# Optimization experiments

Measured on AMD Instinct MI355X. Metric: run time of the kernel, lower is better.

Reference implementation:

```python
import jax, jax.numpy as jnp
import numpy as np

N_NODES = 100000
IN_CH = 256
EMBED = 256
N_EDGES = 300000
EPS = 1e-5


def _glorot(key, shape):
    fan_in, fan_out = shape[0], shape[1]
    lim = (6.0 / (fan_in + fan_out)) ** 0.5
    return jax.random.uniform(key, shape, jnp.float32, -lim, lim)


def setup_inputs() -> dict:
    key = jax.random.key(0)
    ks = jax.random.split(key, 16)
    inp = {}
    inp['node_feat'] = jax.random.normal(ks[0], (N_NODES, IN_CH), jnp.float32)
    inp['src'] = jax.random.randint(ks[1], (N_EDGES,), 0, N_NODES, jnp.int32)
    inp['dst'] = jax.random.randint(ks[2], (N_EDGES,), 0, N_NODES, jnp.int32)
    inp['neg'] = jax.random.randint(ks[3], (N_EDGES,), 0, N_NODES, jnp.int32)
    # GCNConv weights (x @ W + b), 3 layers
    inp['W1'] = _glorot(ks[4], (IN_CH, EMBED)); inp['b1'] = jnp.zeros((EMBED,), jnp.float32)
    inp['W2'] = _glorot(ks[5], (EMBED, EMBED)); inp['b2'] = jnp.zeros((EMBED,), jnp.float32)
    inp['W3'] = _glorot(ks[6], (EMBED, EMBED)); inp['b3'] = jnp.zeros((EMBED,), jnp.float32)
    # BatchNorm affine params (2 BN layers)
    inp['g1'] = jnp.ones((EMBED,), jnp.float32); inp['be1'] = jnp.zeros((EMBED,), jnp.float32)
    inp['g2'] = jnp.ones((EMBED,), jnp.float32); inp['be2'] = jnp.zeros((EMBED,), jnp.float32)
    # LinkPredictor MLP
    inp['fc1_w'] = _glorot(ks[7], (2 * EMBED, EMBED)); inp['fc1_b'] = jnp.zeros((EMBED,), jnp.float32)
    inp['fc2_w'] = _glorot(ks[8], (EMBED, 1)); inp['fc2_b'] = jnp.zeros((1,), jnp.float32)
    return inp


def gcn_conv(x, W, b, src, dst, n):
    # PyG GCNConv: out = D^{-1/2} (A + I) D^{-1/2} (x @ W) + b
    xw = x @ W
    loops = jnp.arange(n, dtype=src.dtype)
    src_l = jnp.concatenate([src, loops])
    dst_l = jnp.concatenate([dst, loops])
    deg = jax.ops.segment_sum(jnp.ones_like(dst_l, jnp.float32), dst_l, num_segments=n)
    dinv = jnp.where(deg > 0, jax.lax.rsqrt(deg), 0.0)
    norm = dinv[src_l] * dinv[dst_l]  # [E+N]
    msg = norm[:, None] * xw[src_l]   # [E+N, d]
    out = jax.ops.segment_sum(msg, dst_l, num_segments=n)
    return out + b


def batch_norm(x, g, b):
    # training-mode BN over node dim, biased variance (torch semantics)
    mu = jnp.mean(x, axis=0)
    var = jnp.mean((x - mu) ** 2, axis=0)
    return (x - mu) * jax.lax.rsqrt(var + EPS) * g + b


def link_pred(z_a, z_b, fc1_w, fc1_b, fc2_w, fc2_b):
    h = jnp.concatenate([z_a, z_b], axis=1) @ fc1_w + fc1_b
    h = jax.nn.relu(h)
    return jax.nn.sigmoid(h @ fc2_w + fc2_b).reshape(-1)


def reference(node_feat, src, dst, neg, W1, b1, W2, b2, W3, b3, g1, be1, g2, be2, fc1_w, fc1_b, fc2_w, fc2_b):
    n = node_feat.shape[0]
    # encoder (dropout p used only in training; inference/deterministic here)
    x = gcn_conv(node_feat, W1, b1, src, dst, n)
    x = jax.nn.relu(batch_norm(x, g1, be1))
    x = gcn_conv(x, W2, b2, src, dst, n)
    x = jax.nn.relu(batch_norm(x, g2, be2))
    z = gcn_conv(x, W3, b3, src, dst, n)
    z_src, z_dst, z_neg = z[src], z[dst], z[neg]
    pos_out = link_pred(z_src, z_dst, fc1_w, fc1_b, fc2_w, fc2_b)
    neg_out = link_pred(z_src, z_neg, fc1_w, fc1_b, fc2_w, fc2_b)
    return (pos_out, neg_out)
```

## Files before the change

### kernel.cpp

```cpp
#include <hip/hip_runtime.h>
#include <hip/hip_bf16.h>

#define N_NODES 100000
#define N_EDGES 300000
#define CH 256
#define EPS 1e-5f
#define AGG_BLOCKS 3125
#define Y_TILES 782
#define Y_TILES_PAD 784

typedef __hip_bfloat16 bf16;
typedef __attribute__((ext_vector_type(8))) short bf16x8_t;
typedef __attribute__((ext_vector_type(4))) float f32x4_t;

__device__ __forceinline__ unsigned short f2bf(float f) {
    bf16 h = __float2bfloat16(f);
    return __builtin_bit_cast(unsigned short, h);
}
__device__ __forceinline__ float bflo(unsigned int w) {
    return __builtin_bit_cast(float, w << 16);
}
__device__ __forceinline__ float bfhi(unsigned int w) {
    return __builtin_bit_cast(float, w & 0xffff0000u);
}
__device__ __forceinline__ unsigned pack2(float a, float b) {
    return (unsigned)f2bf(a) | ((unsigned)f2bf(b) << 16);
}
__device__ __forceinline__ void store_val(bf16* p, float v) { *p = __float2bfloat16(v); }

__device__ __forceinline__ void async_copy16(const void* g, void* l) {
    __builtin_amdgcn_global_load_lds((const __attribute__((address_space(1))) void*)g,
                                     (__attribute__((address_space(3))) void*)l, 16, 0, 0);
}

__global__ void k_zero_int(int* __restrict__ p, int n) {
    int i = blockIdx.x * 256 + threadIdx.x;
    if (i < n) p[i] = 0;
}
__global__ void k_count_deg(const int* __restrict__ dst, int* __restrict__ deg) {
    int e = blockIdx.x * 256 + threadIdx.x;
    if (e < N_EDGES) atomicAdd(&deg[dst[e]], 1);
}
__global__ void k_block_sums(const int* __restrict__ deg, int* __restrict__ bsum,
                             float* __restrict__ dinv) {
    __shared__ int s[256];
    int t = threadIdx.x;
    int i = blockIdx.x * 256 + t;
    int v = (i < N_NODES) ? deg[i] : 0;
    s[t] = v;
    if (i < N_NODES) dinv[i] = rsqrtf((float)(v + 1));
    __syncthreads();
    for (int off = 128; off > 0; off >>= 1) {
        if (t < off) s[t] += s[t + off];
        __syncthreads();
    }
    if (t == 0) bsum[blockIdx.x] = s[0];
}
__global__ void k_scan_bsums(int* __restrict__ bsum, int nb) {
    __shared__ int s[512];
    int t = threadIdx.x;
    int v = (t < nb) ? bsum[t] : 0;
    s[t] = v;
    __syncthreads();
    for (int off = 1; off < 512; off <<= 1) {
        int u = (t >= off) ? s[t - off] : 0;
        __syncthreads();
        s[t] += u;
        __syncthreads();
    }
    if (t < nb) bsum[t] = s[t] - v;
}
__global__ void k_row_ptr(const int* __restrict__ deg, const int* __restrict__ bsum,
                          int* __restrict__ row_ptr) {
    __shared__ int s[256];
    int t = threadIdx.x;
    int i = blockIdx.x * 256 + t;
    int v = (i < N_NODES) ? deg[i] : 0;
    s[t] = v;
    __syncthreads();
    for (int off = 1; off < 256; off <<= 1) {
        int u = (t >= off) ? s[t - off] : 0;
        __syncthreads();
        s[t] += u;
        __syncthreads();
    }
    if (i < N_NODES) row_ptr[i] = bsum[blockIdx.x] + s[t] - v;
    if (blockIdx.x == 0 && t == 0) row_ptr[N_NODES] = N_EDGES;
}
__global__ void k_scatter(const int* __restrict__ src, const int* __restrict__ dst,
                          const int* __restrict__ row_ptr, int* __restrict__ cursor,
                          const float* __restrict__ dinv,
                          int* __restrict__ col, float* __restrict__ wedge,
                          int* __restrict__ eid, int* __restrict__ rowid) {
    int e = blockIdx.x * 256 + threadIdx.x;
    if (e < N_EDGES) {
        int d = dst[e], s = src[e];
        int p = atomicAdd(&cursor[d], 1);
        int idx = row_ptr[d] + p;
        col[idx] = s;
        wedge[idx] = dinv[d] * dinv[s];
        eid[idx] = e;
        rowid[idx] = d;
    }
}

__global__ void k_transpose_all(const float* __restrict__ W1, const float* __restrict__ W2,
                                bf16* __restrict__ wt) {
    int which = blockIdx.x >> 8;
    int idx = ((blockIdx.x & 255) << 8) + threadIdx.x;
    int n = idx >> 8, k = idx & 255;
    const float* W = which ? W2 : W1;
    wt[(size_t)which * 65536 + (size_t)n * 256 + k] =
        __float2bfloat16(W[(size_t)k * 256 + n]);
}

__global__ void k_fuse_w(const float* __restrict__ W3, const float* __restrict__ fc1w,
                         const float* __restrict__ b3, const float* __restrict__ fc1b,
                         bf16* __restrict__ wtf, float* __restrict__ bout) {
    int n = threadIdx.x;
    int nc = n & 255;
    size_t ro = (n < 256) ? 0 : 256;
    if (blockIdx.x == 256) {
        float acc = (n < 256) ? fc1b[n] : 0.f;
#pragma unroll 4
        for (int j = 0; j < 256; ++j)
            acc += b3[j] * fc1w[(ro + j) * 256 + nc];
        bout[n] = acc;
        return;
    }
    __shared__ float w3row[256];
    int k = blockIdx.x;
    if (n < 256) w3row[n] = W3[(size_t)k * 256 + n];
    __syncthreads();
    float acc = 0.f;
#pragma unroll 4
    for (int j = 0; j < 256; ++j)
        acc += w3row[j] * fc1w[(ro + j) * 256 + nc];
    wtf[(size_t)n * 256 + k] = __float2bfloat16(acc);
}

template <int NX, bool BIAS, bool STATS, bool F32A>
__global__ __launch_bounds__(256) void k_gemm_mfma(const bf16* __restrict__ A,
                                                   const float* __restrict__ Af,
                                                   const bf16* __restrict__ Bt,
                                                   bf16* __restrict__ C, int M, int ldc,
                                                   const float* __restrict__ bias,
                                                   float* __restrict__ part) {
    constexpr int LOG2NX = (NX == 4) ? 2 : 1;
    int id = blockIdx.x;
    int rg = (id & 7) + 8 * (id >> (3 + LOG2NX));
    int ct = (id >> 3) & (NX - 1);
    if (rg >= Y_TILES) return;
    const int row0 = rg * 128;
    const int col0 = ct * 128;

    __shared__ bf16 As[128 * 64];
    __shared__ bf16 Bs[128 * 64];
    __shared__ float sS[2][128];
    __shared__ float sQ[2][128];
    const int tid = threadIdx.x;
    const int lane = tid & 63;
    const int w = tid >> 6;
    const int wr = w >> 1, wc = w & 1;
    const int lr = lane & 15, quad = lane >> 4;

    f32x4_t acc[4][4] = {};

    for (int k0 = 0; k0 < 256; k0 += 64) {
#pragma unroll
        for (int i = 0; i < 4; ++i) {
            int j = i * 256 + tid;
            int r = j >> 3, c = j & 7;
            int gk = ((c ^ (r & 7)) << 3);
            int gr = row0 + r; gr = gr < M ? gr : M - 1;
            if (F32A) {
                const float4* ap = (const float4*)(Af + (size_t)gr * 256 + k0 + gk);
                float4 fa = ap[0], fb = ap[1];
                uint4 o;
                o.x = pack2(fa.x, fa.y); o.y = pack2(fa.z, fa.w);
                o.z = pack2(fb.x, fb.y); o.w = pack2(fb.z, fb.w);
                *(uint4*)(As + (size_t)j * 8) = o;
            } else {
                async_copy16(A + (size_t)gr * 256 + k0 + gk, (void*)(As + j * 8));
            }
            async_copy16(Bt + (size_t)(col0 + r) * 256 + k0 + gk, (void*)(Bs + j * 8));
        }
        __syncthreads();
#pragma unroll
        for (int ks = 0; ks < 2; ++ks) {
            bf16x8_t af[4], bfr[4];
#pragma unroll
            for (int mi = 0; mi < 4; ++mi) {
                int m = wr * 64 + mi * 16 + lr;
                int c = (ks * 4 + quad) ^ (m & 7);
                af[mi] = *(const bf16x8_t*)(As + m * 64 + c * 8);
            }
#pragma unroll
            for (int ni = 0; ni < 4; ++ni) {
                int n = wc * 64 + ni * 16 + lr;
                int c = (ks * 4 + quad) ^ (n & 7);
                bfr[ni] = *(const bf16x8_t*)(Bs + n * 64 + c * 8);
            }
#pragma unroll
            for (int mi = 0; mi < 4; ++mi)
#pragma unroll
                for (int ni = 0; ni < 4; ++ni)
                    acc[mi][ni] = __builtin_amdgcn_mfma_f32_16x16x32_bf16(
                        af[mi], bfr[ni], acc[mi][ni], 0, 0, 0);
        }
        __syncthreads();
    }
#pragma unroll
    for (int ni = 0; ni < 4; ++ni) {
        int colg = col0 + wc * 64 + ni * 16 + lr;
        float bv = BIAS ? bias[colg] : 0.f;
#pragma unroll
        for (int mi = 0; mi < 4; ++mi)
#pragma unroll
            for (int r = 0; r < 4; ++r) acc[mi][ni][r] += bv;
    }
    if (STATS) {
        float cs[4] = {}, cq[4] = {};
#pragma unroll
        for (int mi = 0; mi < 4; ++mi)
#pragma unroll
            for (int r = 0; r < 4; ++r) {
                int row = row0 + wr * 64 + mi * 16 + quad * 4 + r;
                if (row < M) {
#pragma unroll
                    for (int ni = 0; ni < 4; ++ni) {
                        float v = acc[mi][ni][r];
                        cs[ni] += v;
                        cq[ni] += v * v;
                    }
                }
            }
#pragma unroll
        for (int ni = 0; ni < 4; ++ni) {
            cs[ni] += __shfl_xor(cs[ni], 16, 64);
            cs[ni] += __shfl_xor(cs[ni], 32, 64);
            cq[ni] += __shfl_xor(cq[ni], 16, 64);
            cq[ni] += __shfl_xor(cq[ni], 32, 64);
        }
        if (quad == 0) {
#pragma unroll
            for (int ni = 0; ni < 4; ++ni) {
                int cc = wc * 64 + ni * 16 + lr;
                sS[wr][cc] = cs[ni];
                sQ[wr][cc] = cq[ni];
            }
        }
        __syncthreads();
        if (tid < 128) {
            float ss = sS[0][tid] + sS[1][tid];
            float qq = sQ[0][tid] + sQ[1][tid];
            int cg = col0 + tid;
            part[(size_t)rg * 512 + cg] = ss;
            part[(size_t)rg * 512 + 256 + cg] = qq;
        }
    }
#pragma unroll
    for (int mi = 0; mi < 4; ++mi) {
#pragma unroll
        for (int r = 0; r < 4; ++r) {
            int row = row0 + wr * 64 + mi * 16 + quad * 4 + r;
            if (row < M) {
#pragma unroll
                for (int ni = 0; ni < 4; ++ni) {
                    int colg = col0 + wc * 64 + ni * 16 + lr;
                    store_val(C + (size_t)row * ldc + colg, acc[mi][ni][r]);
                }
            }
        }
    }
}

template <bool BN>
__device__ __forceinline__ void expand8(uint4 m, const float* sc, const float* sh, float* r) {
    r[0] = bflo(m.x); r[1] = bfhi(m.x); r[2] = bflo(m.y); r[3] = bfhi(m.y);
    r[4] = bflo(m.z); r[5] = bfhi(m.z); r[6] = bflo(m.w); r[7] = bfhi(m.w);
    if (BN) {
#pragma unroll
        for (int i = 0; i < 8; ++i) r[i] = fmaxf(r[i] * sc[i] + sh[i], 0.f);
    }
}

template <bool BN, bool STATS>
__global__ __launch_bounds__(256) void k_agg_csr(const unsigned short* __restrict__ x,
                                                 const int* __restrict__ row_ptr,
                                                 const int* __restrict__ col,
                                                 const float* __restrict__ wedge,
                                                 const float* __restrict__ dinv,
                                                 const float* __restrict__ scale,
                                                 const float* __restrict__ shift,
                                                 const float* __restrict__ bias,
                                                 bf16* __restrict__ out,
                                                 float* __restrict__ part) {
    __shared__ float sred[8][256];
    __shared__ float qred[8][256];
    int g = threadIdx.x >> 5, lh = threadIdx.x & 31;
    int base = blockIdx.x * 32 + g * 4;
    const uint4* xv = (const uint4*)x;
    float sc[8], sh[8], bs[8];
    if (BN) {
        float4 a = ((const float4*)scale)[lh * 2];
        float4 b = ((const float4*)scale)[lh * 2 + 1];
        float4 c = ((const float4*)shift)[lh * 2];
        float4 d = ((const float4*)shift)[lh * 2 + 1];
        sc[0] = a.x; sc[1] = a.y; sc[2] = a.z; sc[3] = a.w;
        sc[4] = b.x; sc[5] = b.y; sc[6] = b.z; sc[7] = b.w;
        sh[0] = c.x; sh[1] = c.y; sh[2] = c.z; sh[3] = c.w;
        sh[4] = d.x; sh[5] = d.y; sh[6] = d.z; sh[7] = d.w;
    }
    if (STATS) {
        float4 e = ((const float4*)bias)[lh * 2];
        float4 f = ((const float4*)bias)[lh * 2 + 1];
        bs[0] = e.x; bs[1] = e.y; bs[2] = e.z; bs[3] = e.w;
        bs[4] = f.x; bs[5] = f.y; bs[6] = f.z; bs[7] = f.w;
    }
    float s8[8] = {}, q8[8] = {};
#pragma unroll
    for (int n = 0; n < 4; ++n) {
        int node = base + n;
        int beg = row_ptr[node], end = row_ptr[node + 1];
        float dv = dinv[node];
        float s2 = dv * dv;
        uint4 xr = xv[(size_t)node * 32 + lh];
        float rs[8];
        expand8<BN>(xr, sc, sh, rs);
        float a[8];
#pragma unroll
        for (int t = 0; t < 8; ++t) a[t] = s2 * rs[t];
        int i = beg;
        for (; i + 2 <= end; i += 2) {
            int sa = col[i], sb = col[i + 1];
            float wa = wedge[i], wb = wedge[i + 1];
            uint4 ma = xv[(size_t)sa * 32 + lh];
            uint4 mb = xv[(size_t)sb * 32 + lh];
            float ra[8], rb[8];
            expand8<BN>(ma, sc, sh, ra);
            expand8<BN>(mb, sc, sh, rb);
#pragma unroll
            for (int t = 0; t < 8; ++t) a[t] += wa * ra[t] + wb * rb[t];
        }
        if (i < end) {
            int sa = col[i];
            float wa = wedge[i];
            uint4 ma = xv[(size_t)sa * 32 + lh];
            float ra[8];
            expand8<BN>(ma, sc, sh, ra);
#pragma unroll
            for (int t = 0; t < 8; ++t) a[t] += wa * ra[t];
        }
        if (STATS) {
#pragma unroll
            for (int t = 0; t < 8; ++t) {
                a[t] += bs[t];
                s8[t] += a[t];
                q8[t] += a[t] * a[t];
            }
        }
        uint4 o;
        o.x = pack2(a[0], a[1]); o.y = pack2(a[2], a[3]);
        o.z = pack2(a[4], a[5]); o.w = pack2(a[6], a[7]);
        ((uint4*)(out + (size_t)node * CH))[lh] = o;
    }
    if (STATS) {
#pragma unroll
        for (int j = 0; j < 8; ++j) {
            sred[g][lh * 8 + j] = s8[j];
            qred[g][lh * 8 + j] = q8[j];
        }
        __syncthreads();
        int t = threadIdx.x;
        float ss = 0.f, qq = 0.f;
#pragma unroll
        for (int gg = 0; gg < 8; ++gg) {
            ss += sred[gg][t];
            qq += qred[gg][t];
        }
        part[(size_t)blockIdx.x * 512 + t] = ss;
        part[(size_t)blockIdx.x * 512 + 256 + t] = qq;
    }
}

__global__ __launch_bounds__(256) void k_bn_finalize(const float* __restrict__ part,
                                                     const float* __restrict__ g,
                                                     const float* __restrict__ be,
                                                     float* __restrict__ scale,
                                                     float* __restrict__ shift, int npart) {
    int wave = threadIdx.x >> 6, lane = threadIdx.x & 63;
    int c = blockIdx.x * 4 + wave;
    float s = 0.f, q = 0.f;
    for (int j = lane; j < npart; j += 64) {
        s += part[(size_t)j * 512 + c];
        q += part[(size_t)j * 512 + 256 + c];
    }
#pragma unroll
    for (int off = 32; off > 0; off >>= 1) {
        s += __shfl_down(s, off, 64);
        q += __shfl_down(q, off, 64);
    }
    if (lane == 0) {
        float mu = s * (1.0f / N_NODES);
        float var = q * (1.0f / N_NODES) - mu * mu;
        float sc = g[c] * rsqrtf(var + EPS);
        scale[c] = sc;
        shift[c] = be[c] - mu * sc;
    }
}

__global__ __launch_bounds__(256) void k_edge_score(
        const unsigned short* __restrict__ uv,
        const int* __restrict__ col, const int* __restrict__ eid,
        const int* __restrict__ rowid, const int* __restrict__ neg,
        const float* __restrict__ fc2_w, const float* __restrict__ fc2_b,
        float* __restrict__ out) {
    constexpr int NWG = 18750;
    constexpr int Q = NWG / 8, R = NWG % 8;
    int bid = blockIdx.x;
    int xcd = bid & 7, ord = bid >> 3;
    int swz = ((xcd < R) ? xcd * (Q + 1) : R * (Q + 1) + (xcd - R) * Q) + ord;
    int wave = threadIdx.x >> 6, lane = threadIdx.x & 63;
    int qtr = lane >> 4, l = lane & 15;
    int i = swz * 16 + wave * 4 + qtr;
    int s = col[i], d = rowid[i], e = eid[i];
    int g = neg[e];
    const uint4* uvv = (const uint4*)uv;
    uint4 u0 = uvv[(size_t)s * 64 + l * 2];
    uint4 u1 = uvv[(size_t)s * 64 + l * 2 + 1];
    uint4 p0 = uvv[(size_t)d * 64 + 32 + l * 2];
    uint4 p1 = uvv[(size_t)d * 64 + 33 + l * 2];
    uint4 n0 = uvv[(size_t)g * 64 + 32 + l * 2];
    uint4 n1 = uvv[(size_t)g * 64 + 33 + l * 2];
    float4 w0 = ((const float4*)fc2_w)[l * 4];
    float4 w1 = ((const float4*)fc2_w)[l * 4 + 1];
    float4 w2 = ((const float4*)fc2_w)[l * 4 + 2];
    float4 w3 = ((const float4*)fc2_w)[l * 4 + 3];

    float t0 = bflo(u0.x), t1 = bfhi(u0.x), t2 = bflo(u0.y), t3 = bfhi(u0.y);
    float t4 = bflo(u0.z), t5 = bfhi(u0.z), t6 = bflo(u0.w), t7 = bfhi(u0.w);
    float t8 = bflo(u1.x), t9 = bfhi(u1.x), ta = bflo(u1.y), tb = bfhi(u1.y);
    float tc = bflo(u1.z), td = bfhi(u1.z), te = bflo(u1.w), tf = bfhi(u1.w);

    float accp =
        fmaxf(t0 + bflo(p0.x), 0.f) * w0.x + fmaxf(t1 + bfhi(p0.x), 0.f) * w0.y +
        fmaxf(t2 + bflo(p0.y), 0.f) * w0.z + fmaxf(t3 + bfhi(p0.y), 0.f) * w0.w +
        fmaxf(t4 + bflo(p0.z), 0.f) * w1.x + fmaxf(t5 + bfhi(p0.z), 0.f) * w1.y +
        fmaxf(t6 + bflo(p0.w), 0.f) * w1.z + fmaxf(t7 + bfhi(p0.w), 0.f) * w1.w +
        fmaxf(t8 + bflo(p1.x), 0.f) * w2.x + fmaxf(t9 + bfhi(p1.x), 0.f) * w2.y +
        fmaxf(ta + bflo(p1.y), 0.f) * w2.z + fmaxf(tb + bfhi(p1.y), 0.f) * w2.w +
        fmaxf(tc + bflo(p1.z), 0.f) * w3.x + fmaxf(td + bfhi(p1.z), 0.f) * w3.y +
        fmaxf(te + bflo(p1.w), 0.f) * w3.z + fmaxf(tf + bfhi(p1.w), 0.f) * w3.w;
    float accn =
        fmaxf(t0 + bflo(n0.x), 0.f) * w0.x + fmaxf(t1 + bfhi(n0.x), 0.f) * w0.y +
        fmaxf(t2 + bflo(n0.y), 0.f) * w0.z + fmaxf(t3 + bfhi(n0.y), 0.f) * w0.w +
        fmaxf(t4 + bflo(n0.z), 0.f) * w1.x + fmaxf(t5 + bfhi(n0.z), 0.f) * w1.y +
        fmaxf(t6 + bflo(n0.w), 0.f) * w1.z + fmaxf(t7 + bfhi(n0.w), 0.f) * w1.w +
        fmaxf(t8 + bflo(n1.x), 0.f) * w2.x + fmaxf(t9 + bfhi(n1.x), 0.f) * w2.y +
        fmaxf(ta + bflo(n1.y), 0.f) * w2.z + fmaxf(tb + bfhi(n1.y), 0.f) * w2.w +
        fmaxf(tc + bflo(n1.z), 0.f) * w3.x + fmaxf(td + bfhi(n1.z), 0.f) * w3.y +
        fmaxf(te + bflo(n1.w), 0.f) * w3.z + fmaxf(tf + bfhi(n1.w), 0.f) * w3.w;
#pragma unroll
    for (int off = 8; off > 0; off >>= 1) {
        accp += __shfl_down(accp, off, 64);
        accn += __shfl_down(accn, off, 64);
    }
    if (l == 0) {
        float bb = fc2_b[0];
        out[e] = 1.0f / (1.0f + expf(-(accp + bb)));
        out[N_EDGES + e] = 1.0f / (1.0f + expf(-(accn + bb)));
    }
}

extern "C" void kernel_launch(void* const* d_in, const int* in_sizes, int n_in,
                              void* d_out, int out_size, void* d_ws, size_t ws_size,
                              hipStream_t stream) {
    const float* node_feat = (const float*)d_in[0];
    const int* src = (const int*)d_in[1];
    const int* dst = (const int*)d_in[2];
    const int* neg = (const int*)d_in[3];
    const float* W1 = (const float*)d_in[4];  const float* b1 = (const float*)d_in[5];
    const float* W2 = (const float*)d_in[6];  const float* b2 = (const float*)d_in[7];
    const float* W3 = (const float*)d_in[8];  const float* b3 = (const float*)d_in[9];
    const float* g1 = (const float*)d_in[10]; const float* be1 = (const float*)d_in[11];
    const float* g2 = (const float*)d_in[12]; const float* be2 = (const float*)d_in[13];
    const float* fc1_w = (const float*)d_in[14]; const float* fc1_b = (const float*)d_in[15];
    const float* fc2_w = (const float*)d_in[16]; const float* fc2_b = (const float*)d_in[17];
    float* out = (float*)d_out;

    const size_t NF = (size_t)N_NODES * CH;
    bf16* UV = (bf16*)d_ws;
    bf16* Xbf = UV + 2 * NF;
    bf16* XwBf = Xbf + NF;
    bf16* wt = XwBf + NF;
    float* dinv = (float*)(wt + 4 * 65536);
    float* bnpart = dinv + N_NODES;
    float* scale = bnpart + (size_t)AGG_BLOCKS * 512;
    float* shift = scale + CH;
    float* b3fc = shift + CH;
    float* wedge = b3fc + 512;
    int* ideg = (int*)(wedge + N_EDGES);
    int* cursor = ideg + N_NODES;
    int* row_ptr = cursor + N_NODES;
    int* col = row_ptr + N_NODES + 1;
    int* eid = col + N_EDGES;
    int* rowid = eid + N_EDGES;
    int* bsum = rowid + N_EDGES;
    (void)ws_size;

    int gemmBlocks = 2 * Y_TILES_PAD;
    int uvBlocks = 4 * Y_TILES_PAD;
    int nodeBlocks = (N_NODES + 255) / 256;
    int edgeBlocks = (N_EDGES + 255) / 256;
    int scoreBlocks = N_EDGES / 16;

    k_zero_int<<<(2 * N_NODES + 255) / 256, 256, 0, stream>>>(ideg, 2 * N_NODES);
    k_count_deg<<<edgeBlocks, 256, 0, stream>>>(dst, ideg);
    k_block_sums<<<nodeBlocks, 256, 0, stream>>>(ideg, bsum, dinv);
    k_scan_bsums<<<1, 512, 0, stream>>>(bsum, nodeBlocks);
    k_row_ptr<<<nodeBlocks, 256, 0, stream>>>(ideg, bsum, row_ptr);
    k_scatter<<<edgeBlocks, 256, 0, stream>>>(src, dst, row_ptr, cursor, dinv, col, wedge,
                                              eid, rowid);

    k_transpose_all<<<512, 256, 0, stream>>>(W1, W2, wt);
    k_fuse_w<<<257, 512, 0, stream>>>(W3, fc1_w, b3, fc1_b, wt + 2 * 65536, b3fc);

    k_gemm_mfma<2, false, false, true><<<gemmBlocks, 256, 0, stream>>>(
        nullptr, node_feat, wt, XwBf, N_NODES, 256, nullptr, nullptr);
    k_agg_csr<false, true><<<AGG_BLOCKS, 256, 0, stream>>>(
        (unsigned short*)XwBf, row_ptr, col, wedge, dinv, nullptr, nullptr, b1, Xbf, bnpart);
    k_bn_finalize<<<64, 256, 0, stream>>>(bnpart, g1, be1, scale, shift, AGG_BLOCKS);

    k_agg_csr<true, false><<<AGG_BLOCKS, 256, 0, stream>>>(
        (unsigned short*)Xbf, row_ptr, col, wedge, dinv, scale, shift, nullptr, XwBf, nullptr);
    k_gemm_mfma<2, true, true, false><<<gemmBlocks, 256, 0, stream>>>(
        XwBf, nullptr, wt + 65536, Xbf, N_NODES, 256, b2, bnpart);
    k_bn_finalize<<<64, 256, 0, stream>>>(bnpart, g2, be2, scale, shift, Y_TILES);

    k_agg_csr<true, false><<<AGG_BLOCKS, 256, 0, stream>>>(
        (unsigned short*)Xbf, row_ptr, col, wedge, dinv, scale, shift, nullptr, XwBf, nullptr);
    k_gemm_mfma<4, true, false, false><<<uvBlocks, 256, 0, stream>>>(
        XwBf, nullptr, wt + 2 * 65536, UV, N_NODES, 512, b3fc, nullptr);

    k_edge_score<<<scoreBlocks, 256, 0, stream>>>((unsigned short*)UV, col, eid, rowid, neg,
                                                  fc2_w, fc2_b, out);
}
```

Baseline: 558.8 us.

## Double-buffer GEMM shared-memory tiles to overlap global loads with MFMA compute

```diff
diff --git a/kernel.cpp b/kernel.cpp
--- a/kernel.cpp
+++ b/kernel.cpp
@@ -154,8 +154,8 @@
     const int row0 = rg * 128;
     const int col0 = ct * 128;
 
-    __shared__ bf16 As[128 * 64];
-    __shared__ bf16 Bs[128 * 64];
+    __shared__ bf16 As[2 * 128 * 64];
+    __shared__ bf16 Bs[2 * 128 * 64];
     __shared__ float sS[2][128];
     __shared__ float sQ[2][128];
     const int tid = threadIdx.x;
@@ -166,26 +166,51 @@
 
     f32x4_t acc[4][4] = {};
 
-    for (int k0 = 0; k0 < 256; k0 += 64) {
+    auto issue_b = [&](int k0, int buf) {
+#pragma unroll
+        for (int i = 0; i < 4; ++i) {
+            int j = i * 256 + tid;
+            int r = j >> 3, c = j & 7;
+            int gk = ((c ^ (r & 7)) << 3);
+            async_copy16(Bt + (size_t)(col0 + r) * 256 + k0 + gk,
+                         (void*)(Bs + buf * 8192 + j * 8));
+        }
+    };
+    auto issue_a = [&](int k0, int buf) {
 #pragma unroll
         for (int i = 0; i < 4; ++i) {
             int j = i * 256 + tid;
             int r = j >> 3, c = j & 7;
             int gk = ((c ^ (r & 7)) << 3);
             int gr = row0 + r; gr = gr < M ? gr : M - 1;
-            if (F32A) {
-                const float4* ap = (const float4*)(Af + (size_t)gr * 256 + k0 + gk);
-                float4 fa = ap[0], fb = ap[1];
-                uint4 o;
-                o.x = pack2(fa.x, fa.y); o.y = pack2(fa.z, fa.w);
-                o.z = pack2(fb.x, fb.y); o.w = pack2(fb.z, fb.w);
-                *(uint4*)(As + (size_t)j * 8) = o;
-            } else {
-                async_copy16(A + (size_t)gr * 256 + k0 + gk, (void*)(As + j * 8));
-            }
-            async_copy16(Bt + (size_t)(col0 + r) * 256 + k0 + gk, (void*)(Bs + j * 8));
-        }
-        __syncthreads();
+            async_copy16(A + (size_t)gr * 256 + k0 + gk, (void*)(As + buf * 8192 + j * 8));
+        }
+    };
+    auto load_a = [&](int k0, float4* rr) {
+#pragma unroll
+        for (int i = 0; i < 4; ++i) {
+            int j = i * 256 + tid;
+            int r = j >> 3, c = j & 7;
+            int gk = ((c ^ (r & 7)) << 3);
+            int gr = row0 + r; gr = gr < M ? gr : M - 1;
+            const float4* ap = (const float4*)(Af + (size_t)gr * 256 + k0 + gk);
+            rr[2 * i] = ap[0];
+            rr[2 * i + 1] = ap[1];
+        }
+    };
+    auto write_a = [&](const float4* rr, int buf) {
+#pragma unroll
+        for (int i = 0; i < 4; ++i) {
+            int j = i * 256 + tid;
+            uint4 o;
+            o.x = pack2(rr[2 * i].x, rr[2 * i].y);
+            o.y = pack2(rr[2 * i].z, rr[2 * i].w);
+            o.z = pack2(rr[2 * i + 1].x, rr[2 * i + 1].y);
+            o.w = pack2(rr[2 * i + 1].z, rr[2 * i + 1].w);
+            *(uint4*)(As + buf * 8192 + (size_t)j * 8) = o;
+        }
+    };
+    auto compute = [&](int buf) {
 #pragma unroll
         for (int ks = 0; ks < 2; ++ks) {
             bf16x8_t af[4], bfr[4];
@@ -193,13 +218,13 @@
             for (int mi = 0; mi < 4; ++mi) {
                 int m = wr * 64 + mi * 16 + lr;
                 int c = (ks * 4 + quad) ^ (m & 7);
-                af[mi] = *(const bf16x8_t*)(As + m * 64 + c * 8);
+                af[mi] = *(const bf16x8_t*)(As + buf * 8192 + m * 64 + c * 8);
             }
 #pragma unroll
             for (int ni = 0; ni < 4; ++ni) {
                 int n = wc * 64 + ni * 16 + lr;
                 int c = (ks * 4 + quad) ^ (n & 7);
-                bfr[ni] = *(const bf16x8_t*)(Bs + n * 64 + c * 8);
+                bfr[ni] = *(const bf16x8_t*)(Bs + buf * 8192 + n * 64 + c * 8);
             }
 #pragma unroll
             for (int mi = 0; mi < 4; ++mi)
@@ -208,8 +233,42 @@
                     acc[mi][ni] = __builtin_amdgcn_mfma_f32_16x16x32_bf16(
                         af[mi], bfr[ni], acc[mi][ni], 0, 0, 0);
         }
-        __syncthreads();
-    }
+    };
+
+    float4 pre0[8], pre1[8];
+    if constexpr (F32A) { issue_b(0, 0); load_a(0, pre0); }
+    else { issue_a(0, 0); issue_b(0, 0); }
+
+#pragma unroll
+    for (int k = 0; k < 4; ++k) {
+        const int cur = k & 1;
+        if constexpr (F32A) {
+            if (k == 0) { issue_b(64, 1); load_a(64, pre1); }
+            else if (k == 1) { issue_b(128, 0); load_a(128, pre0); }
+            else if (k == 2) { issue_b(192, 1); load_a(192, pre1); }
+        } else {
+            if (k < 3) { issue_a((k + 1) * 64, cur ^ 1); issue_b((k + 1) * 64, cur ^ 1); }
+        }
+        __builtin_amdgcn_sched_barrier(0);
+        if (k < 3) {
+            if constexpr (F32A) asm volatile("s_waitcnt vmcnt(12)" ::: "memory");
+            else asm volatile("s_waitcnt vmcnt(8)" ::: "memory");
+        } else {
+            asm volatile("s_waitcnt vmcnt(0)" ::: "memory");
+        }
+        __builtin_amdgcn_sched_barrier(0);
+        if constexpr (F32A) {
+            if (k == 0 || k == 2) write_a(pre0, cur);
+            else write_a(pre1, cur);
+            asm volatile("s_waitcnt lgkmcnt(0)" ::: "memory");
+            __builtin_amdgcn_sched_barrier(0);
+        }
+        __builtin_amdgcn_s_barrier();
+        compute(cur);
+        __builtin_amdgcn_s_barrier();
+        __builtin_amdgcn_sched_barrier(0);
+    }
+
 #pragma unroll
     for (int ni = 0; ni < 4; ++ni) {
         int colg = col0 + wc * 64 + ni * 16 + lr;
```

Measured after the change: 565.7 us. No clear change (+1.2%).

## Double-buffer GEMM LDS loads and overlap fp32-to-bf16 cast with graph preprocessing

Applied to the files above, without the earlier changes.

```diff
diff --git a/kernel.cpp b/kernel.cpp
--- a/kernel.cpp
+++ b/kernel.cpp
@@ -8,6 +8,7 @@
 #define AGG_BLOCKS 3125
 #define Y_TILES 782
 #define Y_TILES_PAD 784
+#define CAST_CHUNK 5000
 
 typedef __hip_bfloat16 bf16;
 typedef __attribute__((ext_vector_type(8))) short bf16x8_t;
@@ -33,16 +34,42 @@
                                      (__attribute__((address_space(3))) void*)l, 16, 0, 0);
 }
 
-__global__ void k_zero_int(int* __restrict__ p, int n) {
+__device__ __forceinline__ void cast_chunk(const float* __restrict__ x,
+                                           unsigned short* __restrict__ y, int i) {
+    float4 v = ((const float4*)x)[i];
+    ushort4 o;
+    o.x = f2bf(v.x); o.y = f2bf(v.y); o.z = f2bf(v.z); o.w = f2bf(v.w);
+    ((ushort4*)y)[i] = o;
+}
+
+__global__ void k_zero_int(int* __restrict__ p, int n,
+                           const float* __restrict__ cx, unsigned short* __restrict__ cy,
+                           int castBase, int nbMain) {
+    if ((int)blockIdx.x >= nbMain) {
+        cast_chunk(cx, cy, (castBase + (int)blockIdx.x - nbMain) * 256 + (int)threadIdx.x);
+        return;
+    }
     int i = blockIdx.x * 256 + threadIdx.x;
     if (i < n) p[i] = 0;
 }
-__global__ void k_count_deg(const int* __restrict__ dst, int* __restrict__ deg) {
+__global__ void k_count_deg(const int* __restrict__ dst, int* __restrict__ deg,
+                            const float* __restrict__ cx, unsigned short* __restrict__ cy,
+                            int castBase, int nbMain) {
+    if ((int)blockIdx.x >= nbMain) {
+        cast_chunk(cx, cy, (castBase + (int)blockIdx.x - nbMain) * 256 + (int)threadIdx.x);
+        return;
+    }
     int e = blockIdx.x * 256 + threadIdx.x;
     if (e < N_EDGES) atomicAdd(&deg[dst[e]], 1);
 }
 __global__ void k_block_sums(const int* __restrict__ deg, int* __restrict__ bsum,
-                             float* __restrict__ dinv) {
+                             float* __restrict__ dinv,
+                             const float* __restrict__ cx, unsigned short* __restrict__ cy,
+                             int castBase, int nbMain) {
+    if ((int)blockIdx.x >= nbMain) {
+        cast_chunk(cx, cy, (castBase + (int)blockIdx.x - nbMain) * 256 + (int)threadIdx.x);
+        return;
+    }
     __shared__ int s[256];
     int t = threadIdx.x;
     int i = blockIdx.x * 256 + t;
@@ -71,7 +98,13 @@
     if (t < nb) bsum[t] = s[t] - v;
 }
 __global__ void k_row_ptr(const int* __restrict__ deg, const int* __restrict__ bsum,
-                          int* __restrict__ row_ptr) {
+                          int* __restrict__ row_ptr,
+                          const float* __restrict__ cx, unsigned short* __restrict__ cy,
+                          int castBase, int nbMain) {
+    if ((int)blockIdx.x >= nbMain) {
+        cast_chunk(cx, cy, (castBase + (int)blockIdx.x - nbMain) * 256 + (int)threadIdx.x);
+        return;
+    }
     __shared__ int s[256];
     int t = threadIdx.x;
     int i = blockIdx.x * 256 + t;
@@ -91,7 +124,13 @@
                           const int* __restrict__ row_ptr, int* __restrict__ cursor,
                           const float* __restrict__ dinv,
                           int* __restrict__ col, float* __restrict__ wedge,
-                          int* __restrict__ eid, int* __restrict__ rowid) {
+                          int* __restrict__ eid, int* __restrict__ rowid,
+                          const float* __restrict__ cx, unsigned short* __restrict__ cy,
+                          int castBase, int nbMain) {
+    if ((int)blockIdx.x >= nbMain) {
+        cast_chunk(cx, cy, (castBase + (int)blockIdx.x - nbMain) * 256 + (int)threadIdx.x);
+        return;
+    }
     int e = blockIdx.x * 256 + threadIdx.x;
     if (e < N_EDGES) {
         int d = dst[e], s = src[e];
@@ -139,9 +178,8 @@
     wtf[(size_t)n * 256 + k] = __float2bfloat16(acc);
 }
 
-template <int NX, bool BIAS, bool STATS, bool F32A>
+template <int NX, bool BIAS, bool STATS>
 __global__ __launch_bounds__(256) void k_gemm_mfma(const bf16* __restrict__ A,
-                                                   const float* __restrict__ Af,
                                                    const bf16* __restrict__ Bt,
                                                    bf16* __restrict__ C, int M, int ldc,
                                                    const float* __restrict__ bias,
@@ -154,8 +192,8 @@
     const int row0 = rg * 128;
     const int col0 = ct * 128;
 
-    __shared__ bf16 As[128 * 64];
-    __shared__ bf16 Bs[128 * 64];
+    __shared__ bf16 As[2 * 128 * 64];
+    __shared__ bf16 Bs[2 * 128 * 64];
     __shared__ float sS[2][128];
     __shared__ float sQ[2][128];
     const int tid = threadIdx.x;
@@ -166,26 +204,19 @@
 
     f32x4_t acc[4][4] = {};
 
-    for (int k0 = 0; k0 < 256; k0 += 64) {
+    auto issue_ab = [&](int k0, int buf) {
 #pragma unroll
         for (int i = 0; i < 4; ++i) {
             int j = i * 256 + tid;
             int r = j >> 3, c = j & 7;
             int gk = ((c ^ (r & 7)) << 3);
             int gr = row0 + r; gr = gr < M ? gr : M - 1;
-            if (F32A) {
-                const float4* ap = (const float4*)(Af + (size_t)gr * 256 + k0 + gk);
-                float4 fa = ap[0], fb = ap[1];
-                uint4 o;
-                o.x = pack2(fa.x, fa.y); o.y = pack2(fa.z, fa.w);
-                o.z = pack2(fb.x, fb.y); o.w = pack2(fb.z, fb.w);
-                *(uint4*)(As + (size_t)j * 8) = o;
-            } else {
-                async_copy16(A + (size_t)gr * 256 + k0 + gk, (void*)(As + j * 8));
-            }
-            async_copy16(Bt + (size_t)(col0 + r) * 256 + k0 + gk, (void*)(Bs + j * 8));
-        }
-        __syncthreads();
+            async_copy16(A + (size_t)gr * 256 + k0 + gk, (void*)(As + buf * 8192 + j * 8));
+            async_copy16(Bt + (size_t)(col0 + r) * 256 + k0 + gk,
+                         (void*)(Bs + buf * 8192 + j * 8));
+        }
+    };
+    auto compute = [&](int buf) {
 #pragma unroll
         for (int ks = 0; ks < 2; ++ks) {
             bf16x8_t af[4], bfr[4];
@@ -193,13 +224,13 @@
             for (int mi = 0; mi < 4; ++mi) {
                 int m = wr * 64 + mi * 16 + lr;
                 int c = (ks * 4 + quad) ^ (m & 7);
-                af[mi] = *(const bf16x8_t*)(As + m * 64 + c * 8);
+                af[mi] = *(const bf16x8_t*)(As + buf * 8192 + m * 64 + c * 8);
             }
 #pragma unroll
             for (int ni = 0; ni < 4; ++ni) {
                 int n = wc * 64 + ni * 16 + lr;
                 int c = (ks * 4 + quad) ^ (n & 7);
-                bfr[ni] = *(const bf16x8_t*)(Bs + n * 64 + c * 8);
+                bfr[ni] = *(const bf16x8_t*)(Bs + buf * 8192 + n * 64 + c * 8);
             }
 #pragma unroll
             for (int mi = 0; mi < 4; ++mi)
@@ -208,8 +239,24 @@
                     acc[mi][ni] = __builtin_amdgcn_mfma_f32_16x16x32_bf16(
                         af[mi], bfr[ni], acc[mi][ni], 0, 0, 0);
         }
-        __syncthreads();
-    }
+    };
+
+    issue_ab(0, 0);
+
+#pragma unroll
+    for (int k = 0; k < 4; ++k) {
+        const int cur = k & 1;
+        if (k < 3) issue_ab((k + 1) * 64, cur ^ 1);
+        __builtin_amdgcn_sched_barrier(0);
+        if (k < 3) asm volatile("s_waitcnt vmcnt(8)" ::: "memory");
+        else asm volatile("s_waitcnt vmcnt(0)" ::: "memory");
+        __builtin_amdgcn_sched_barrier(0);
+        __builtin_amdgcn_s_barrier();
+        compute(cur);
+        __builtin_amdgcn_s_barrier();
+        __builtin_amdgcn_sched_barrier(0);
+    }
+
 #pragma unroll
     for (int ni = 0; ni < 4; ++ni) {
         int colg = col0 + wc * 64 + ni * 16 + lr;
@@ -513,35 +560,42 @@
     int uvBlocks = 4 * Y_TILES_PAD;
     int nodeBlocks = (N_NODES + 255) / 256;
     int edgeBlocks = (N_EDGES + 255) / 256;
+    int zeroBlocks = (2 * N_NODES + 255) / 256;
     int scoreBlocks = N_EDGES / 16;
-
-    k_zero_int<<<(2 * N_NODES + 255) / 256, 256, 0, stream>>>(ideg, 2 * N_NODES);
-    k_count_deg<<<edgeBlocks, 256, 0, stream>>>(dst, ideg);
-    k_block_sums<<<nodeBlocks, 256, 0, stream>>>(ideg, bsum, dinv);
+    unsigned short* Xc = (unsigned short*)Xbf;
+
+    k_zero_int<<<zeroBlocks + CAST_CHUNK, 256, 0, stream>>>(
+        ideg, 2 * N_NODES, node_feat, Xc, 0 * CAST_CHUNK, zeroBlocks);
+    k_count_deg<<<edgeBlocks + CAST_CHUNK, 256, 0, stream>>>(
+        dst, ideg, node_feat, Xc, 1 * CAST_CHUNK, edgeBlocks);
+    k_block_sums<<<nodeBlocks + CAST_CHUNK, 256, 0, stream>>>(
+        ideg, bsum, dinv, node_feat, Xc, 2 * CAST_CHUNK, nodeBlocks);
     k_scan_bsums<<<1, 512, 0, stream>>>(bsum, nodeBlocks);
-    k_row_ptr<<<nodeBlocks, 256, 0, stream>>>(ideg, bsum, row_ptr);
-    k_scatter<<<edgeBlocks, 256, 0, stream>>>(src, dst, row_ptr, cursor, dinv, col, wedge,
-                                              eid, rowid);
+    k_row_ptr<<<nodeBlocks + CAST_CHUNK, 256, 0, stream>>>(
+        ideg, bsum, row_ptr, node_feat, Xc, 3 * CAST_CHUNK, nodeBlocks);
+    k_scatter<<<edgeBlocks + CAST_CHUNK, 256, 0, stream>>>(
+        src, dst, row_ptr, cursor, dinv, col, wedge, eid, rowid,
+        node_feat, Xc, 4 * CAST_CHUNK, edgeBlocks);
 
     k_transpose_all<<<512, 256, 0, stream>>>(W1, W2, wt);
     k_fuse_w<<<257, 512, 0, stream>>>(W3, fc1_w, b3, fc1_b, wt + 2 * 65536, b3fc);
 
-    k_gemm_mfma<2, false, false, true><<<gemmBlocks, 256, 0, stream>>>(
-        nullptr, node_feat, wt, XwBf, N_NODES, 256, nullptr, nullptr);
+    k_gemm_mfma<2, false, false><<<gemmBlocks, 256, 0, stream>>>(
+        Xbf, wt, XwBf, N_NODES, 256, nullptr, nullptr);
     k_agg_csr<false, true><<<AGG_BLOCKS, 256, 0, stream>>>(
         (unsigned short*)XwBf, row_ptr, col, wedge, dinv, nullptr, nullptr, b1, Xbf, bnpart);
     k_bn_finalize<<<64, 256, 0, stream>>>(bnpart, g1, be1, scale, shift, AGG_BLOCKS);
 
     k_agg_csr<true, false><<<AGG_BLOCKS, 256, 0, stream>>>(
         (unsigned short*)Xbf, row_ptr, col, wedge, dinv, scale, shift, nullptr, XwBf, nullptr);
-    k_gemm_mfma<2, true, true, false><<<gemmBlocks, 256, 0, stream>>>(
-        XwBf, nullptr, wt + 65536, Xbf, N_NODES, 256, b2, bnpart);
+    k_gemm_mfma<2, true, true><<<gemmBlocks, 256, 0, stream>>>(
+        XwBf, wt + 65536, Xbf, N_NODES, 256, b2, bnpart);
     k_bn_finalize<<<64, 256, 0, stream>>>(bnpart, g2, be2, scale, shift, Y_TILES);
 
     k_agg_csr<true, false><<<AGG_BLOCKS, 256, 0, stream>>>(
         (unsigned short*)Xbf, row_ptr, col, wedge, dinv, scale, shift, nullptr, XwBf, nullptr);
-    k_gemm_mfma<4, true, false, false><<<uvBlocks, 256, 0, stream>>>(
-        XwBf, nullptr, wt + 2 * 65536, UV, N_NODES, 512, b3fc, nullptr);
+    k_gemm_mfma<4, true, false><<<uvBlocks, 256, 0, stream>>>(
+        XwBf, wt + 2 * 65536, UV, N_NODES, 512, b3fc, nullptr);
 
     k_edge_score<<<scoreBlocks, 256, 0, stream>>>((unsigned short*)UV, col, eid, rowid, neg,
                                                   fc2_w, fc2_b, out);
```

Measured after the change: 575.8 us. 3.0% more time.
